# Kernel optimization log

Measured on AMD Instinct MI355X. Metric: run time of the kernel, lower is better.

The kernel has to match this reference:

```python
import jax, jax.numpy as jnp
import numpy as np

DIM = 512
HEADS = 8

def setup_inputs() -> dict:
    key = jax.random.key(0)
    ks = jax.random.split(key, 24)
    B, Nq, N3, N4, D = 8, 4096, 1024, 256, DIM
    def lin(k):
        k1, k2 = jax.random.split(k)
        s = 1.0 / np.sqrt(D)
        return (jax.random.uniform(k1, (D, D), jnp.float32, -s, s),
                jax.random.uniform(k2, (D,), jnp.float32, -s, s))
    Wq1, bq1 = lin(ks[0]); Wk1, bk1 = lin(ks[1]); Wv1, bv1 = lin(ks[2])
    Wq2, bq2 = lin(ks[3]); Wk2, bk2 = lin(ks[4]); Wv2, bv2 = lin(ks[5])
    sr = 1.0 / np.sqrt(2 * D)
    Wr = jax.random.uniform(ks[6], (D, 2 * D), jnp.float32, -sr, sr)
    br = jax.random.uniform(ks[7], (D,), jnp.float32, -sr, sr)
    return {
        'f2': jax.random.normal(ks[8], (B, Nq, D), jnp.float32),
        'f3': jax.random.normal(ks[9], (B, N3, D), jnp.float32),
        'f4': jax.random.normal(ks[10], (B, N4, D), jnp.float32),
        'f2_pos_embed': jax.random.normal(ks[11], (B, Nq, D), jnp.float32),
        'f3_pos_embed': jax.random.normal(ks[12], (B, N3, D), jnp.float32),
        'f4_pos_embed': jax.random.normal(ks[13], (B, N4, D), jnp.float32),
        'Wq1': Wq1, 'bq1': bq1, 'Wk1': Wk1, 'bk1': bk1, 'Wv1': Wv1, 'bv1': bv1,
        'Wq2': Wq2, 'bq2': bq2, 'Wk2': Wk2, 'bk2': bk2, 'Wv2': Wv2, 'bv2': bv2,
        'Wr': Wr, 'br': br,
    }

def _linear(x, W, b):
    return x @ W.T + b

def _efficient_branch(q, k, v, H):
    # q: [B,Nq,D], k/v: [B,Nk,D]. Split D into H heads of dh channels (contiguous).
    B, Nq, D = q.shape
    Nk = k.shape[1]
    dh = D // H
    q = q.reshape(B, Nq, H, dh)
    k = k.reshape(B, Nk, H, dh)
    v = v.reshape(B, Nk, H, dh)
    qs = jax.nn.softmax(q, axis=1)   # softmax over query positions (torch dim=2 in [B,C,N])
    ks = jax.nn.softmax(k, axis=3)   # softmax over head key channels (torch dim=1)
    # context[b,h,d,e] = sum_n ks[b,n,h,d] * v[b,n,h,e]  -> [B,H,dh,dh]
    context = jnp.einsum('bnhd,bnhe->bhde', ks, v)
    # attended[b,n,h,e] = sum_d context[b,h,d,e] * qs[b,n,h,d]
    attended = jnp.einsum('bhde,bnhd->bnhe', context, qs)
    return attended.reshape(B, Nq, D)

def reference(f2, f3, f4, f2_pos_embed, f3_pos_embed, f4_pos_embed,
              Wq1, bq1, Wk1, bk1, Wv1, bv1,
              Wq2, bq2, Wk2, bk2, Wv2, bv2, Wr, br):
    f2p = f2 + f2_pos_embed
    q1 = _linear(f2p, Wq1, bq1)
    q2 = _linear(f2p, Wq2, bq2)
    k3 = _linear(f3 + f3_pos_embed, Wk1, bk1)
    v3 = _linear(f3, Wv1, bv1)
    k4 = _linear(f4 + f4_pos_embed, Wk2, bk2)
    v4 = _linear(f4, Wv2, bv2)
    agg32 = _efficient_branch(q1, k3, v3, HEADS)  # [B,Nq,D]
    agg42 = _efficient_branch(q2, k4, v4, HEADS)  # [B,Nq,D]
    out = jnp.concatenate([agg32, agg42], axis=-1)
    return _linear(out, Wr, br)  # dropout p=0 -> identity
```

## Files before the change

### kernel.cpp

```cpp
#include <hip/hip_runtime.h>

typedef unsigned short ushort_t;
typedef unsigned int uint32;
typedef __attribute__((ext_vector_type(8))) short short8;
typedef __attribute__((ext_vector_type(4))) float f32x4;

static __device__ __forceinline__ ushort_t f2bf(float f) {
  uint32 u = __builtin_bit_cast(uint32, f);
  u += 0x7fffu + ((u >> 16) & 1u);
  return (ushort_t)(u >> 16);
}
static __device__ __forceinline__ float bf2f(ushort_t h) {
  return __builtin_bit_cast(float, (uint32)h << 16);
}

static __device__ __forceinline__ void gload_lds16(const ushort_t* g, ushort_t* l) {
  __builtin_amdgcn_global_load_lds(
      (const __attribute__((address_space(1))) uint32*)g,
      (__attribute__((address_space(3))) uint32*)l, 16, 0, 0);
}

static __device__ __forceinline__ void addcvt4(const float* __restrict__ a,
                                               const float* __restrict__ b,
                                               ushort_t* __restrict__ o, int i) {
  float4 va = reinterpret_cast<const float4*>(a)[i];
  if (b != nullptr) {
    float4 vb = reinterpret_cast<const float4*>(b)[i];
    va.x += vb.x; va.y += vb.y; va.z += vb.z; va.w += vb.w;
  }
  ushort4 u;
  u.x = f2bf(va.x); u.y = f2bf(va.y); u.z = f2bf(va.z); u.w = f2bf(va.w);
  reinterpret_cast<ushort4*>(o)[i] = u;
}

static __device__ __forceinline__ void ctx_block(
    const ushort_t* __restrict__ ks3, const ushort_t* __restrict__ v3,
    const ushort_t* __restrict__ ks4, const ushort_t* __restrict__ v4,
    float* __restrict__ ctxOut, int cb, ushort_t* sm) {
  ushort_t (*ks_s)[68] = reinterpret_cast<ushort_t(*)[68]>(sm);
  ushort_t (*v_s)[68] = reinterpret_cast<ushort_t(*)[68]>(sm + 4352);
  const int t = threadIdx.x;
  const ushort_t* ks; const ushort_t* v; float* dstBase; int Nk, bh, chunk;
  if (cb < 256) { ks = ks3; v = v3; dstBase = ctxOut;          Nk = 1024; bh = cb >> 2; chunk = cb & 3; }
  else          { ks = ks4; v = v4; dstBase = ctxOut + 262144; Nk = 256;  bh = cb - 256; chunk = 0; }
  const int bb = bh >> 3, h = bh & 7;
  const int td = t & 15, te = t >> 4;
  float acc[4][4] = {};
  size_t rowBase = (size_t)bb * Nk + chunk * 256;
  for (int n0 = 0; n0 < 256; n0 += 64) {
#pragma unroll
    for (int i = 0; i < 4; i++) {
      int idx = i * 256 + t;
      int n = idx >> 4, dq = idx & 15;
      size_t g = (rowBase + n0 + n) * 512 + h * 64 + dq * 4;
      *reinterpret_cast<ushort4*>(&ks_s[n][dq * 4]) = *reinterpret_cast<const ushort4*>(ks + g);
      *reinterpret_cast<ushort4*>(&v_s[n][dq * 4]) = *reinterpret_cast<const ushort4*>(v + g);
    }
    __syncthreads();
#pragma unroll 8
    for (int n = 0; n < 64; n++) {
      ushort4 cu = *reinterpret_cast<const ushort4*>(&ks_s[n][td * 4]);
      ushort4 vu = *reinterpret_cast<const ushort4*>(&v_s[n][te * 4]);
      float ca[4] = {bf2f(cu.x), bf2f(cu.y), bf2f(cu.z), bf2f(cu.w)};
      float va[4] = {bf2f(vu.x), bf2f(vu.y), bf2f(vu.z), bf2f(vu.w)};
#pragma unroll
      for (int i = 0; i < 4; i++)
#pragma unroll
        for (int j = 0; j < 4; j++) acc[i][j] += ca[i] * va[j];
    }
    __syncthreads();
  }
  float* dst = dstBase + (size_t)bh * 4096;
#pragma unroll
  for (int i = 0; i < 4; i++)
#pragma unroll
    for (int j = 0; j < 4; j++)
      atomicAdd(&dst[(td * 4 + i) * 64 + te * 4 + j], acc[i][j]);
}

__global__ void prepA_kernel(const float* __restrict__ f3, const float* __restrict__ f3pe,
                             const float* __restrict__ f4, const float* __restrict__ f4pe,
                             const float* __restrict__ Wq1, const float* __restrict__ Wq2,
                             const float* __restrict__ Wk1, const float* __restrict__ Wv1,
                             const float* __restrict__ Wk2, const float* __restrict__ Wv2,
                             const float* __restrict__ bq1, const float* __restrict__ bq2,
                             ushort_t* __restrict__ f3p, ushort_t* __restrict__ f3b,
                             ushort_t* __restrict__ f4p, ushort_t* __restrict__ f4b,
                             ushort_t* __restrict__ WqB, ushort_t* __restrict__ Wk1B,
                             ushort_t* __restrict__ Wv1B, ushort_t* __restrict__ Wk2B,
                             ushort_t* __restrict__ Wv2B, float* __restrict__ bqc,
                             float* __restrict__ Z, float* __restrict__ ctx) {
  int b = blockIdx.x, t = threadIdx.x;
  if (b < 4096) {
    int i = b * 256 + t;
    float4 va = reinterpret_cast<const float4*>(f3)[i];
    float4 vp = reinterpret_cast<const float4*>(f3pe)[i];
    ushort4 ub, up;
    ub.x = f2bf(va.x); ub.y = f2bf(va.y); ub.z = f2bf(va.z); ub.w = f2bf(va.w);
    up.x = f2bf(va.x + vp.x); up.y = f2bf(va.y + vp.y);
    up.z = f2bf(va.z + vp.z); up.w = f2bf(va.w + vp.w);
    reinterpret_cast<ushort4*>(f3b)[i] = ub;
    reinterpret_cast<ushort4*>(f3p)[i] = up;
  } else if (b < 5120) {
    int i = (b - 4096) * 256 + t;
    float4 va = reinterpret_cast<const float4*>(f4)[i];
    float4 vp = reinterpret_cast<const float4*>(f4pe)[i];
    ushort4 ub, up;
    ub.x = f2bf(va.x); ub.y = f2bf(va.y); ub.z = f2bf(va.z); ub.w = f2bf(va.w);
    up.x = f2bf(va.x + vp.x); up.y = f2bf(va.y + vp.y);
    up.z = f2bf(va.z + vp.z); up.w = f2bf(va.w + vp.w);
    reinterpret_cast<ushort4*>(f4b)[i] = ub;
    reinterpret_cast<ushort4*>(f4p)[i] = up;
  } else if (b < 6656) {
    int u = b - 5120;
    int arr = u >> 8, i = (u & 255) * 256 + t;
    const float* s; ushort_t* d;
    switch (arr) {
      case 0: s = Wq1; d = WqB; break;
      case 1: s = Wq2; d = WqB + 262144; break;
      case 2: s = Wk1; d = Wk1B; break;
      case 3: s = Wv1; d = Wv1B; break;
      case 4: s = Wk2; d = Wk2B; break;
      default: s = Wv2; d = Wv2B; break;
    }
    addcvt4(s, nullptr, d, i);
  } else if (b < 7168) {
    reinterpret_cast<float4*>(ctx)[(b - 6656) * 256 + t] = make_float4(0.f, 0.f, 0.f, 0.f);
  } else {
    for (int i = t; i < 512; i += 256) { bqc[i] = bq1[i]; bqc[512 + i] = bq2[i]; }
    for (int i = t; i < 8192; i += 256) Z[i] = 0.f;
  }
}

static __device__ __forceinline__ void gemm_core(
    const ushort_t* __restrict__ A, const ushort_t* __restrict__ Bt,
    int K, int mBase, int nBase, ushort_t* As, ushort_t* Bs, f32x4 acc[4][4]) {
  const int t = threadIdx.x;
  const int w = t >> 6, l = t & 63;
  const int l15 = l & 15, l4 = l >> 4;
  const int rowInSeg = l >> 3;
  const int srcOff = ((l & 7) ^ rowInSeg) << 3;
  const int wm = (w >> 1) * 64, wn = (w & 1) * 64;

  for (int k0 = 0; k0 < K; k0 += 64) {
#pragma unroll
    for (int i = 0; i < 4; i++) {
      int seg = w * 4 + i;
      int row = seg * 8 + rowInSeg;
      gload_lds16(A + (size_t)(mBase + row) * K + k0 + srcOff, As + seg * 512);
      gload_lds16(Bt + (size_t)(nBase + row) * K + k0 + srcOff, Bs + seg * 512);
    }
    __syncthreads();
#pragma unroll
    for (int kk = 0; kk < 2; kk++) {
      short8 af[4], bfr[4];
      const int kb = kk * 64 + l4 * 16;
#pragma unroll
      for (int f = 0; f < 4; f++) {
        int rowA = wm + f * 16 + l15;
        af[f] = *reinterpret_cast<const short8*>(
            reinterpret_cast<const char*>(As) + rowA * 128 + (kb ^ ((rowA & 7) << 4)));
        int rowB = wn + f * 16 + l15;
        bfr[f] = *reinterpret_cast<const short8*>(
            reinterpret_cast<const char*>(Bs) + rowB * 128 + (kb ^ ((rowB & 7) << 4)));
      }
#pragma unroll
      for (int fm = 0; fm < 4; fm++)
#pragma unroll
        for (int fn = 0; fn < 4; fn++)
          acc[fm][fn] = __builtin_amdgcn_mfma_f32_16x16x32_bf16(af[fm], bfr[fn], acc[fm][fn], 0, 0, 0);
    }
    __syncthreads();
  }
}

__global__ __launch_bounds__(256, 4)
void gemm_g1(const ushort_t* __restrict__ A, const ushort_t* __restrict__ Bt,
             const float* __restrict__ bias, ushort_t* __restrict__ E,
             float* __restrict__ Z,
             const ushort_t* __restrict__ ks3, const ushort_t* __restrict__ v3,
             const ushort_t* __restrict__ ks4, const ushort_t* __restrict__ v4,
             float* __restrict__ ctx, int ctxBlocks) {
  __shared__ ushort_t smem[16384];
  if ((int)blockIdx.x < ctxBlocks) {
    ctx_block(ks3, v3, ks4, v4, ctx, blockIdx.x, smem);
    return;
  }
  ushort_t* As = smem;
  ushort_t* Bs = smem + 8192;
  const int bid = blockIdx.x - ctxBlocks;
  const int swz = (bid & 7) * 256 + (bid >> 3);
  const int mBase = (swz >> 3) * 128, nBase = (swz & 7) * 128;
  const int t = threadIdx.x, w = t >> 6, lane = t & 63;
  const int l15 = lane & 15, l4 = lane >> 4;
  const int wm = (w >> 1) * 64, wn = (w & 1) * 64;

  f32x4 acc[4][4];
#pragma unroll
  for (int i = 0; i < 4; i++)
#pragma unroll
    for (int j = 0; j < 4; j++) acc[i][j] = (f32x4){0.f, 0.f, 0.f, 0.f};

  gemm_core(A, Bt, 512, mBase, nBase, As, Bs, acc);

  const int N = 1024;
  float bcol[4], csum[4] = {0.f, 0.f, 0.f, 0.f};
#pragma unroll
  for (int fn = 0; fn < 4; fn++) bcol[fn] = bias[nBase + wn + fn * 16 + l15];
#pragma unroll
  for (int fm = 0; fm < 4; fm++) {
#pragma unroll
    for (int r = 0; r < 4; r++) {
      int row = mBase + wm + fm * 16 + l4 * 4 + r;
      float ex[4];
#pragma unroll
      for (int fn = 0; fn < 4; fn++) {
        ex[fn] = __expf(acc[fm][fn][r] + bcol[fn]);
        csum[fn] += ex[fn];
      }
#pragma unroll
      for (int fn = 0; fn < 4; fn++)
        E[(size_t)row * N + nBase + wn + fn * 16 + l15] = f2bf(ex[fn]);
    }
  }
#pragma unroll
  for (int fn = 0; fn < 4; fn++) {
    float s = csum[fn];
    s += __shfl_xor(s, 16);
    s += __shfl_xor(s, 32);
    if (l4 == 0) atomicAdd(&Z[(mBase >> 12) * 1024 + nBase + wn + fn * 16 + l15], s);
  }
}

__global__ __launch_bounds__(256, 4)
void kv_quad(const ushort_t* __restrict__ f3p, const ushort_t* __restrict__ f3b,
             const ushort_t* __restrict__ f4p, const ushort_t* __restrict__ f4b,
             const ushort_t* __restrict__ Wk1B, const ushort_t* __restrict__ Wv1B,
             const ushort_t* __restrict__ Wk2B, const ushort_t* __restrict__ Wv2B,
             const float* __restrict__ bk1, const float* __restrict__ bv1,
             const float* __restrict__ bk2, const float* __restrict__ bv2,
             ushort_t* __restrict__ ks3, ushort_t* __restrict__ v3,
             ushort_t* __restrict__ ks4, ushort_t* __restrict__ v4,
             const float* __restrict__ f2, const float* __restrict__ f2pe,
             ushort_t* __restrict__ f2p) {
  __shared__ ushort_t As[8192], Bs[8192];
  const int bid = blockIdx.x;
  if (bid >= 640) {
    const int base = (bid - 640) * 2048;
    const float4* A4 = reinterpret_cast<const float4*>(f2);
    const float4* P4 = reinterpret_cast<const float4*>(f2pe);
    const int t = threadIdx.x;
#pragma unroll
    for (int half = 0; half < 2; half++) {
      float4 a[4], p[4];
#pragma unroll
      for (int j = 0; j < 4; j++) {
        int i = base + (half * 4 + j) * 256 + t;
        a[j] = A4[i];
        p[j] = P4[i];
      }
#pragma unroll
      for (int j = 0; j < 4; j++) {
        int i = base + (half * 4 + j) * 256 + t;
        ushort4 u;
        u.x = f2bf(a[j].x + p[j].x); u.y = f2bf(a[j].y + p[j].y);
        u.z = f2bf(a[j].z + p[j].z); u.w = f2bf(a[j].w + p[j].w);
        reinterpret_cast<ushort4*>(f2p)[i] = u;
      }
    }
    return;
  }
  const int id = (bid & 7) * 80 + (bid >> 3);
  const ushort_t* A; const ushort_t* Bt; const float* bias; ushort_t* out;
  bool doSM; int loc;
  if (id < 256)      { A = f3p; Bt = Wk1B; bias = bk1; out = ks3; doSM = true;  loc = id; }
  else if (id < 512) { A = f3b; Bt = Wv1B; bias = bv1; out = v3;  doSM = false; loc = id - 256; }
  else if (id < 576) { A = f4p; Bt = Wk2B; bias = bk2; out = ks4; doSM = true;  loc = id - 512; }
  else               { A = f4b; Bt = Wv2B; bias = bv2; out = v4;  doSM = false; loc = id - 576; }
  const int nBase = (loc & 3) * 128, mBase = (loc >> 2) * 128;
  const int t = threadIdx.x, w = t >> 6, lane = t & 63;
  const int l15 = lane & 15, l4 = lane >> 4;
  const int wm = (w >> 1) * 64, wn = (w & 1) * 64;

  f32x4 acc[4][4];
#pragma unroll
  for (int i = 0; i < 4; i++)
#pragma unroll
    for (int j = 0; j < 4; j++) acc[i][j] = (f32x4){0.f, 0.f, 0.f, 0.f};

  gemm_core(A, Bt, 512, mBase, nBase, As, Bs, acc);

  const int N = 512;
  float bcol[4];
#pragma unroll
  for (int fn = 0; fn < 4; fn++) bcol[fn] = bias[nBase + wn + fn * 16 + l15];

  if (doSM) {
#pragma unroll
    for (int fm = 0; fm < 4; fm++) {
#pragma unroll
      for (int r = 0; r < 4; r++) {
        float x[4], m = -1e30f;
#pragma unroll
        for (int fn = 0; fn < 4; fn++) { x[fn] = acc[fm][fn][r] + bcol[fn]; m = fmaxf(m, x[fn]); }
        m = fmaxf(m, __shfl_xor(m, 1));
        m = fmaxf(m, __shfl_xor(m, 2));
        m = fmaxf(m, __shfl_xor(m, 4));
        m = fmaxf(m, __shfl_xor(m, 8));
        float s = 0.f;
#pragma unroll
        for (int fn = 0; fn < 4; fn++) { x[fn] = __expf(x[fn] - m); s += x[fn]; }
        s += __shfl_xor(s, 1);
        s += __shfl_xor(s, 2);
        s += __shfl_xor(s, 4);
        s += __shfl_xor(s, 8);
        float inv = 1.f / s;
        int row = mBase + wm + fm * 16 + l4 * 4 + r;
#pragma unroll
        for (int fn = 0; fn < 4; fn++)
          out[(size_t)row * N + nBase + wn + fn * 16 + l15] = f2bf(x[fn] * inv);
      }
    }
  } else {
#pragma unroll
    for (int fm = 0; fm < 4; fm++) {
#pragma unroll
      for (int r = 0; r < 4; r++) {
        int row = mBase + wm + fm * 16 + l4 * 4 + r;
#pragma unroll
        for (int fn = 0; fn < 4; fn++)
          out[(size_t)row * N + nBase + wn + fn * 16 + l15] =
              f2bf(acc[fm][fn][r] + bcol[fn]);
      }
    }
  }
}

__global__ __launch_bounds__(256)
void ctxprepB_kernel(const ushort_t* __restrict__ ks3, const ushort_t* __restrict__ v3,
                     const ushort_t* __restrict__ ks4, const ushort_t* __restrict__ v4,
                     float* __restrict__ ctxOut,
                     const float* __restrict__ f2, const float* __restrict__ f2pe,
                     ushort_t* __restrict__ f2p) {
  __shared__ ushort_t sm[8704];
  const int b = blockIdx.x, t = threadIdx.x;
  if (b >= 320) {
    const int base = (b - 320) * 1024;
    const float4* A4 = reinterpret_cast<const float4*>(f2);
    const float4* P4 = reinterpret_cast<const float4*>(f2pe);
#pragma unroll
    for (int j = 0; j < 4; j++) {
      int i = base + j * 256 + t;
      float4 a = A4[i], p = P4[i];
      ushort4 u;
      u.x = f2bf(a.x + p.x); u.y = f2bf(a.y + p.y);
      u.z = f2bf(a.z + p.z); u.w = f2bf(a.w + p.w);
      reinterpret_cast<ushort4*>(f2p)[i] = u;
    }
    return;
  }
  ctx_block(ks3, v3, ks4, v4, ctxOut, b, sm);
}

__global__ __launch_bounds__(256, 4)
void gemm_g2(const ushort_t* __restrict__ E, const ushort_t* __restrict__ Mt,
             const float* __restrict__ bias, float* __restrict__ C) {
  __shared__ ushort_t As[8192], Bs[8192];
  const int bid = blockIdx.x;
  const int swz = (bid & 7) * 128 + (bid >> 3);
  const int tx = swz & 3, ty = swz >> 2;
  const int mBase = ty * 128, nBase = tx * 128;
  const ushort_t* Btb = Mt + (size_t)(ty >> 5) * 524288;
  const int t = threadIdx.x, w = t >> 6, lane = t & 63;
  const int l15 = lane & 15, l4 = lane >> 4;
  const int wm = (w >> 1) * 64, wn = (w & 1) * 64;

  f32x4 acc[4][4];
#pragma unroll
  for (int i = 0; i < 4; i++)
#pragma unroll
    for (int j = 0; j < 4; j++) acc[i][j] = (f32x4){0.f, 0.f, 0.f, 0.f};

  gemm_core(E, Btb, 1024, mBase, nBase, As, Bs, acc);

  const int N = 512;
  float bcol[4];
#pragma unroll
  for (int fn = 0; fn < 4; fn++) bcol[fn] = bias[nBase + wn + fn * 16 + l15];
#pragma unroll
  for (int fm = 0; fm < 4; fm++) {
#pragma unroll
    for (int r = 0; r < 4; r++) {
      int row = mBase + wm + fm * 16 + l4 * 4 + r;
#pragma unroll
      for (int fn = 0; fn < 4; fn++)
        C[(size_t)row * N + nBase + wn + fn * 16 + l15] = acc[fm][fn][r] + bcol[fn];
    }
  }
}

__global__ __launch_bounds__(256)
void fold_kernel(const float* __restrict__ ctx, const float* __restrict__ Wr,
                 const float* __restrict__ Z, ushort_t* __restrict__ Mt) {
  __shared__ float ctxT[64][68];
  __shared__ float wrT[64][68];
  __shared__ float zinv[64];
  int blk = blockIdx.x;
  int jc = blk & 7;
  int h = (blk >> 3) & 7;
  int branch = (blk >> 6) & 1;
  int b = blk >> 7;
  int t = threadIdx.x;
  int cbase = branch * 512 + h * 64;
  const float* csrc = ctx + (size_t)(branch * 64 + b * 8 + h) * 4096;
#pragma unroll
  for (int i = 0; i < 16; i++) {
    int idx = i * 256 + t;
    int d = idx >> 6, e = idx & 63;
    ctxT[e][d] = csrc[d * 64 + e];
  }
#pragma unroll
  for (int i = 0; i < 16; i++) {
    int idx = i * 256 + t;
    int jl = idx >> 6, e = idx & 63;
    wrT[e][jl] = Wr[(size_t)(jc * 64 + jl) * 1024 + cbase + e];
  }
  if (t < 64) zinv[t] = 1.0f / Z[b * 1024 + cbase + t];
  __syncthreads();
  int td = t & 15, tj = t >> 4;
  float acc[4][4] = {};
#pragma unroll 8
  for (int e = 0; e < 64; e++) {
    float4 cv = *reinterpret_cast<const float4*>(&ctxT[e][td * 4]);
    float4 wv = *reinterpret_cast<const float4*>(&wrT[e][tj * 4]);
    float ca[4] = {cv.x, cv.y, cv.z, cv.w};
    float wa[4] = {wv.x, wv.y, wv.z, wv.w};
#pragma unroll
    for (int i = 0; i < 4; i++)
#pragma unroll
      for (int jj = 0; jj < 4; jj++) acc[i][jj] += ca[i] * wa[jj];
  }
  float zi[4] = {zinv[td * 4], zinv[td * 4 + 1], zinv[td * 4 + 2], zinv[td * 4 + 3]};
#pragma unroll
  for (int jj = 0; jj < 4; jj++) {
    ushort4 u;
    u.x = f2bf(acc[0][jj] * zi[0]);
    u.y = f2bf(acc[1][jj] * zi[1]);
    u.z = f2bf(acc[2][jj] * zi[2]);
    u.w = f2bf(acc[3][jj] * zi[3]);
    *reinterpret_cast<ushort4*>(
        &Mt[(size_t)(b * 512 + jc * 64 + tj * 4 + jj) * 1024 + cbase + td * 4]) = u;
  }
}

extern "C" void kernel_launch(void* const* d_in, const int* in_sizes, int n_in,
                              void* d_out, int out_size, void* d_ws, size_t ws_size,
                              hipStream_t stream) {
  const float* f2 = (const float*)d_in[0];
  const float* f3 = (const float*)d_in[1];
  const float* f4 = (const float*)d_in[2];
  const float* f2pe = (const float*)d_in[3];
  const float* f3pe = (const float*)d_in[4];
  const float* f4pe = (const float*)d_in[5];
  const float* Wq1 = (const float*)d_in[6];
  const float* bq1 = (const float*)d_in[7];
  const float* Wk1 = (const float*)d_in[8];
  const float* bk1 = (const float*)d_in[9];
  const float* Wv1 = (const float*)d_in[10];
  const float* bv1 = (const float*)d_in[11];
  const float* Wq2 = (const float*)d_in[12];
  const float* bq2 = (const float*)d_in[13];
  const float* Wk2 = (const float*)d_in[14];
  const float* bk2 = (const float*)d_in[15];
  const float* Wv2 = (const float*)d_in[16];
  const float* bv2 = (const float*)d_in[17];
  const float* Wr = (const float*)d_in[18];
  const float* br = (const float*)d_in[19];

  char* ws = (char*)d_ws;
  ushort_t* E = (ushort_t*)(ws + 0);
  char* R1 = ws + 67108864;
  ushort_t* f3p = (ushort_t*)R1;
  ushort_t* f3b = (ushort_t*)(R1 + 8388608);
  ushort_t* f4p = (ushort_t*)(R1 + 16777216);
  ushort_t* f4b = (ushort_t*)(R1 + 18874368);
  char* R2 = ws + 100663296;
  ushort_t* ks3 = (ushort_t*)R2;
  ushort_t* v3b = (ushort_t*)(R2 + 8388608);
  ushort_t* ks4 = (ushort_t*)(R2 + 16777216);
  ushort_t* v4b = (ushort_t*)(R2 + 18874368);
  char* R3 = ws + 121634816;
  ushort_t* WqB = (ushort_t*)R3;
  ushort_t* Wk1B = (ushort_t*)(R3 + 1048576);
  ushort_t* Wv1B = (ushort_t*)(R3 + 1572864);
  ushort_t* Wk2B = (ushort_t*)(R3 + 2097152);
  ushort_t* Wv2B = (ushort_t*)(R3 + 2621440);
  ushort_t* Mt = (ushort_t*)(R3 + 3145728);
  float* Z = (float*)(R3 + 11534336);
  float* bqc = (float*)(R3 + 11567104);
  float* ctx = (float*)(R3 + 11571200);
  const bool bigWS = ws_size >= (size_t)176160768;
  ushort_t* f2p = bigWS ? (ushort_t*)(ws + 142606336) : (ushort_t*)R1;

  prepA_kernel<<<7169, 256, 0, stream>>>(f3, f3pe, f4, f4pe,
                                         Wq1, Wq2, Wk1, Wv1, Wk2, Wv2, bq1, bq2,
                                         f3p, f3b, f4p, f4b,
                                         WqB, Wk1B, Wv1B, Wk2B, Wv2B, bqc, Z, ctx);

  if (bigWS) {
    kv_quad<<<2688, 256, 0, stream>>>(f3p, f3b, f4p, f4b,
                                      Wk1B, Wv1B, Wk2B, Wv2B,
                                      bk1, bv1, bk2, bv2,
                                      ks3, v3b, ks4, v4b, f2, f2pe, f2p);
    gemm_g1<<<2368, 256, 0, stream>>>(f2p, WqB, bqc, E, Z,
                                      ks3, v3b, ks4, v4b, ctx, 320);
  } else {
    kv_quad<<<640, 256, 0, stream>>>(f3p, f3b, f4p, f4b,
                                     Wk1B, Wv1B, Wk2B, Wv2B,
                                     bk1, bv1, bk2, bv2,
                                     ks3, v3b, ks4, v4b, f2, f2pe, f2p);
    ctxprepB_kernel<<<4416, 256, 0, stream>>>(ks3, v3b, ks4, v4b, ctx, f2, f2pe, f2p);
    gemm_g1<<<2048, 256, 0, stream>>>(f2p, WqB, bqc, E, Z,
                                      ks3, v3b, ks4, v4b, ctx, 0);
  }

  fold_kernel<<<1024, 256, 0, stream>>>(ctx, Wr, Z, Mt);

  gemm_g2<<<1024, 256, 0, stream>>>(E, Mt, br, (float*)d_out);
}
```

Measured before the change: 175.6 us.

## Replace ctx atomics with per-chunk partial buffers reduced in fold kernel

```diff
diff --git a/kernel.cpp b/kernel.cpp
--- a/kernel.cpp
+++ b/kernel.cpp
@@ -20,29 +20,35 @@
       (__attribute__((address_space(3))) uint32*)l, 16, 0, 0);
 }
 
-static __device__ __forceinline__ void addcvt4(const float* __restrict__ a,
-                                               const float* __restrict__ b,
-                                               ushort_t* __restrict__ o, int i) {
-  float4 va = reinterpret_cast<const float4*>(a)[i];
-  if (b != nullptr) {
-    float4 vb = reinterpret_cast<const float4*>(b)[i];
-    va.x += vb.x; va.y += vb.y; va.z += vb.z; va.w += vb.w;
-  }
+static __device__ __forceinline__ ushort4 cvt4(float4 v) {
   ushort4 u;
-  u.x = f2bf(va.x); u.y = f2bf(va.y); u.z = f2bf(va.z); u.w = f2bf(va.w);
-  reinterpret_cast<ushort4*>(o)[i] = u;
+  u.x = f2bf(v.x); u.y = f2bf(v.y); u.z = f2bf(v.z); u.w = f2bf(v.w);
+  return u;
+}
+static __device__ __forceinline__ ushort4 cvt4s(float4 a, float4 b) {
+  ushort4 u;
+  u.x = f2bf(a.x + b.x); u.y = f2bf(a.y + b.y);
+  u.z = f2bf(a.z + b.z); u.w = f2bf(a.w + b.w);
+  return u;
 }
 
 static __device__ __forceinline__ void ctx_block(
     const ushort_t* __restrict__ ks3, const ushort_t* __restrict__ v3,
     const ushort_t* __restrict__ ks4, const ushort_t* __restrict__ v4,
-    float* __restrict__ ctxOut, int cb, ushort_t* sm) {
+    float* __restrict__ ctxP, int cb, ushort_t* sm) {
   ushort_t (*ks_s)[68] = reinterpret_cast<ushort_t(*)[68]>(sm);
   ushort_t (*v_s)[68] = reinterpret_cast<ushort_t(*)[68]>(sm + 4352);
   const int t = threadIdx.x;
-  const ushort_t* ks; const ushort_t* v; float* dstBase; int Nk, bh, chunk;
-  if (cb < 256) { ks = ks3; v = v3; dstBase = ctxOut;          Nk = 1024; bh = cb >> 2; chunk = cb & 3; }
-  else          { ks = ks4; v = v4; dstBase = ctxOut + 262144; Nk = 256;  bh = cb - 256; chunk = 0; }
+  const ushort_t* ks; const ushort_t* v; float* dst; int Nk, bh, chunk;
+  if (cb < 256) {
+    bh = cb >> 2; chunk = cb & 3;
+    ks = ks3; v = v3; Nk = 1024;
+    dst = ctxP + (size_t)((bh << 2) + chunk) * 4096;
+  } else {
+    bh = cb - 256; chunk = 0;
+    ks = ks4; v = v4; Nk = 256;
+    dst = ctxP + 1048576 + (size_t)bh * 4096;
+  }
   const int bb = bh >> 3, h = bh & 7;
   const int td = t & 15, te = t >> 4;
   float acc[4][4] = {};
@@ -70,12 +76,11 @@
     }
     __syncthreads();
   }
-  float* dst = dstBase + (size_t)bh * 4096;
-#pragma unroll
-  for (int i = 0; i < 4; i++)
-#pragma unroll
-    for (int j = 0; j < 4; j++)
-      atomicAdd(&dst[(td * 4 + i) * 64 + te * 4 + j], acc[i][j]);
+#pragma unroll
+  for (int i = 0; i < 4; i++) {
+    float4 o = make_float4(acc[i][0], acc[i][1], acc[i][2], acc[i][3]);
+    *reinterpret_cast<float4*>(&dst[(td * 4 + i) * 64 + te * 4]) = o;
+  }
 }
 
 __global__ void prepA_kernel(const float* __restrict__ f3, const float* __restrict__ f3pe,
@@ -89,31 +94,29 @@
                              ushort_t* __restrict__ WqB, ushort_t* __restrict__ Wk1B,
                              ushort_t* __restrict__ Wv1B, ushort_t* __restrict__ Wk2B,
                              ushort_t* __restrict__ Wv2B, float* __restrict__ bqc,
-                             float* __restrict__ Z, float* __restrict__ ctx) {
+                             float* __restrict__ Z) {
   int b = blockIdx.x, t = threadIdx.x;
-  if (b < 4096) {
-    int i = b * 256 + t;
-    float4 va = reinterpret_cast<const float4*>(f3)[i];
-    float4 vp = reinterpret_cast<const float4*>(f3pe)[i];
-    ushort4 ub, up;
-    ub.x = f2bf(va.x); ub.y = f2bf(va.y); ub.z = f2bf(va.z); ub.w = f2bf(va.w);
-    up.x = f2bf(va.x + vp.x); up.y = f2bf(va.y + vp.y);
-    up.z = f2bf(va.z + vp.z); up.w = f2bf(va.w + vp.w);
-    reinterpret_cast<ushort4*>(f3b)[i] = ub;
-    reinterpret_cast<ushort4*>(f3p)[i] = up;
-  } else if (b < 5120) {
-    int i = (b - 4096) * 256 + t;
-    float4 va = reinterpret_cast<const float4*>(f4)[i];
-    float4 vp = reinterpret_cast<const float4*>(f4pe)[i];
-    ushort4 ub, up;
-    ub.x = f2bf(va.x); ub.y = f2bf(va.y); ub.z = f2bf(va.z); ub.w = f2bf(va.w);
-    up.x = f2bf(va.x + vp.x); up.y = f2bf(va.y + vp.y);
-    up.z = f2bf(va.z + vp.z); up.w = f2bf(va.w + vp.w);
-    reinterpret_cast<ushort4*>(f4b)[i] = ub;
-    reinterpret_cast<ushort4*>(f4p)[i] = up;
-  } else if (b < 6656) {
-    int u = b - 5120;
-    int arr = u >> 8, i = (u & 255) * 256 + t;
+  if (b < 2048) {
+    int i0 = b * 512 + t, i1 = i0 + 256;
+    const float4* A4 = reinterpret_cast<const float4*>(f3);
+    const float4* P4 = reinterpret_cast<const float4*>(f3pe);
+    float4 a0 = A4[i0], a1 = A4[i1], p0 = P4[i0], p1 = P4[i1];
+    reinterpret_cast<ushort4*>(f3b)[i0] = cvt4(a0);
+    reinterpret_cast<ushort4*>(f3b)[i1] = cvt4(a1);
+    reinterpret_cast<ushort4*>(f3p)[i0] = cvt4s(a0, p0);
+    reinterpret_cast<ushort4*>(f3p)[i1] = cvt4s(a1, p1);
+  } else if (b < 2560) {
+    int i0 = (b - 2048) * 512 + t, i1 = i0 + 256;
+    const float4* A4 = reinterpret_cast<const float4*>(f4);
+    const float4* P4 = reinterpret_cast<const float4*>(f4pe);
+    float4 a0 = A4[i0], a1 = A4[i1], p0 = P4[i0], p1 = P4[i1];
+    reinterpret_cast<ushort4*>(f4b)[i0] = cvt4(a0);
+    reinterpret_cast<ushort4*>(f4b)[i1] = cvt4(a1);
+    reinterpret_cast<ushort4*>(f4p)[i0] = cvt4s(a0, p0);
+    reinterpret_cast<ushort4*>(f4p)[i1] = cvt4s(a1, p1);
+  } else if (b < 3328) {
+    int u = b - 2560;
+    int arr = u >> 7, i0 = (u & 127) * 512 + t, i1 = i0 + 256;
     const float* s; ushort_t* d;
     switch (arr) {
       case 0: s = Wq1; d = WqB; break;
@@ -123,9 +126,10 @@
       case 4: s = Wk2; d = Wk2B; break;
       default: s = Wv2; d = Wv2B; break;
     }
-    addcvt4(s, nullptr, d, i);
-  } else if (b < 7168) {
-    reinterpret_cast<float4*>(ctx)[(b - 6656) * 256 + t] = make_float4(0.f, 0.f, 0.f, 0.f);
+    const float4* S4 = reinterpret_cast<const float4*>(s);
+    float4 v0 = S4[i0], v1 = S4[i1];
+    reinterpret_cast<ushort4*>(d)[i0] = cvt4(v0);
+    reinterpret_cast<ushort4*>(d)[i1] = cvt4(v1);
   } else {
     for (int i = t; i < 512; i += 256) { bqc[i] = bq1[i]; bqc[512 + i] = bq2[i]; }
     for (int i = t; i < 8192; i += 256) Z[i] = 0.f;
@@ -180,15 +184,15 @@
              float* __restrict__ Z,
              const ushort_t* __restrict__ ks3, const ushort_t* __restrict__ v3,
              const ushort_t* __restrict__ ks4, const ushort_t* __restrict__ v4,
-             float* __restrict__ ctx, int ctxBlocks) {
+             float* __restrict__ ctxP, int gemmBlocks) {
   __shared__ ushort_t smem[16384];
-  if ((int)blockIdx.x < ctxBlocks) {
-    ctx_block(ks3, v3, ks4, v4, ctx, blockIdx.x, smem);
+  if ((int)blockIdx.x >= gemmBlocks) {
+    ctx_block(ks3, v3, ks4, v4, ctxP, blockIdx.x - gemmBlocks, smem);
     return;
   }
   ushort_t* As = smem;
   ushort_t* Bs = smem + 8192;
-  const int bid = blockIdx.x - ctxBlocks;
+  const int bid = blockIdx.x;
   const int swz = (bid & 7) * 256 + (bid >> 3);
   const int mBase = (swz >> 3) * 128, nBase = (swz & 7) * 128;
   const int t = threadIdx.x, w = t >> 6, lane = t & 63;
@@ -262,10 +266,7 @@
 #pragma unroll
       for (int j = 0; j < 4; j++) {
         int i = base + (half * 4 + j) * 256 + t;
-        ushort4 u;
-        u.x = f2bf(a[j].x + p[j].x); u.y = f2bf(a[j].y + p[j].y);
-        u.z = f2bf(a[j].z + p[j].z); u.w = f2bf(a[j].w + p[j].w);
-        reinterpret_cast<ushort4*>(f2p)[i] = u;
+        reinterpret_cast<ushort4*>(f2p)[i] = cvt4s(a[j], p[j]);
       }
     }
     return;
@@ -339,7 +340,7 @@
 __global__ __launch_bounds__(256)
 void ctxprepB_kernel(const ushort_t* __restrict__ ks3, const ushort_t* __restrict__ v3,
                      const ushort_t* __restrict__ ks4, const ushort_t* __restrict__ v4,
-                     float* __restrict__ ctxOut,
+                     float* __restrict__ ctxP,
                      const float* __restrict__ f2, const float* __restrict__ f2pe,
                      ushort_t* __restrict__ f2p) {
   __shared__ ushort_t sm[8704];
@@ -352,14 +353,11 @@
     for (int j = 0; j < 4; j++) {
       int i = base + j * 256 + t;
       float4 a = A4[i], p = P4[i];
-      ushort4 u;
-      u.x = f2bf(a.x + p.x); u.y = f2bf(a.y + p.y);
-      u.z = f2bf(a.z + p.z); u.w = f2bf(a.w + p.w);
-      reinterpret_cast<ushort4*>(f2p)[i] = u;
+      reinterpret_cast<ushort4*>(f2p)[i] = cvt4s(a, p);
     }
     return;
   }
-  ctx_block(ks3, v3, ks4, v4, ctxOut, b, sm);
+  ctx_block(ks3, v3, ks4, v4, ctxP, b, sm);
 }
 
 __global__ __launch_bounds__(256, 4)
@@ -400,7 +398,7 @@
 }
 
 __global__ __launch_bounds__(256)
-void fold_kernel(const float* __restrict__ ctx, const float* __restrict__ Wr,
+void fold_kernel(const float* __restrict__ ctxP, const float* __restrict__ Wr,
                  const float* __restrict__ Z, ushort_t* __restrict__ Mt) {
   __shared__ float ctxT[64][68];
   __shared__ float wrT[64][68];
@@ -412,12 +410,23 @@
   int b = blk >> 7;
   int t = threadIdx.x;
   int cbase = branch * 512 + h * 64;
-  const float* csrc = ctx + (size_t)(branch * 64 + b * 8 + h) * 4096;
-#pragma unroll
-  for (int i = 0; i < 16; i++) {
-    int idx = i * 256 + t;
-    int d = idx >> 6, e = idx & 63;
-    ctxT[e][d] = csrc[d * 64 + e];
+  if (branch == 0) {
+    const float* p = ctxP + (size_t)((b * 8 + h) * 4) * 4096;
+#pragma unroll
+    for (int i = 0; i < 16; i++) {
+      int idx = i * 256 + t;
+      int d = idx >> 6, e = idx & 63;
+      int o = d * 64 + e;
+      ctxT[e][d] = p[o] + p[4096 + o] + p[8192 + o] + p[12288 + o];
+    }
+  } else {
+    const float* p = ctxP + 1048576 + (size_t)(b * 8 + h) * 4096;
+#pragma unroll
+    for (int i = 0; i < 16; i++) {
+      int idx = i * 256 + t;
+      int d = idx >> 6, e = idx & 63;
+      ctxT[e][d] = p[d * 64 + e];
+    }
   }
 #pragma unroll
   for (int i = 0; i < 16; i++) {
@@ -498,14 +507,14 @@
   ushort_t* Mt = (ushort_t*)(R3 + 3145728);
   float* Z = (float*)(R3 + 11534336);
   float* bqc = (float*)(R3 + 11567104);
-  float* ctx = (float*)(R3 + 11571200);
+  float* ctxP = (float*)(R3 + 11571200);
   const bool bigWS = ws_size >= (size_t)176160768;
   ushort_t* f2p = bigWS ? (ushort_t*)(ws + 142606336) : (ushort_t*)R1;
 
-  prepA_kernel<<<7169, 256, 0, stream>>>(f3, f3pe, f4, f4pe,
+  prepA_kernel<<<3329, 256, 0, stream>>>(f3, f3pe, f4, f4pe,
                                          Wq1, Wq2, Wk1, Wv1, Wk2, Wv2, bq1, bq2,
                                          f3p, f3b, f4p, f4b,
-                                         WqB, Wk1B, Wv1B, Wk2B, Wv2B, bqc, Z, ctx);
+                                         WqB, Wk1B, Wv1B, Wk2B, Wv2B, bqc, Z);
 
   if (bigWS) {
     kv_quad<<<2688, 256, 0, stream>>>(f3p, f3b, f4p, f4b,
@@ -513,18 +522,18 @@
                                       bk1, bv1, bk2, bv2,
                                       ks3, v3b, ks4, v4b, f2, f2pe, f2p);
     gemm_g1<<<2368, 256, 0, stream>>>(f2p, WqB, bqc, E, Z,
-                                      ks3, v3b, ks4, v4b, ctx, 320);
+                                      ks3, v3b, ks4, v4b, ctxP, 2048);
   } else {
     kv_quad<<<640, 256, 0, stream>>>(f3p, f3b, f4p, f4b,
                                      Wk1B, Wv1B, Wk2B, Wv2B,
                                      bk1, bv1, bk2, bv2,
                                      ks3, v3b, ks4, v4b, f2, f2pe, f2p);
-    ctxprepB_kernel<<<4416, 256, 0, stream>>>(ks3, v3b, ks4, v4b, ctx, f2, f2pe, f2p);
+    ctxprepB_kernel<<<4416, 256, 0, stream>>>(ks3, v3b, ks4, v4b, ctxP, f2, f2pe, f2p);
     gemm_g1<<<2048, 256, 0, stream>>>(f2p, WqB, bqc, E, Z,
-                                      ks3, v3b, ks4, v4b, ctx, 0);
-  }
-
-  fold_kernel<<<1024, 256, 0, stream>>>(ctx, Wr, Z, Mt);
+                                      ks3, v3b, ks4, v4b, ctxP, 2048);
+  }
+
+  fold_kernel<<<1024, 256, 0, stream>>>(ctxP, Wr, Z, Mt);
 
   gemm_g2<<<1024, 256, 0, stream>>>(E, Mt, br, (float*)d_out);
 }
```

New measurement: 177.8 us. About the same (+1.2%).
